# Optimization experiments

Hardware: AMD Instinct MI355X
Metric: run time of the kernel (lower is better)

Reference implementation:

```python
import jax, jax.numpy as jnp
import numpy as np

B, S, D, H = 4, 2048, 1024, 16
DH = D // H


def setup_inputs() -> dict:
    key = jax.random.key(0)
    k1, k2, k3, k4, k5 = jax.random.split(key, 5)
    x = jax.random.normal(k1, (B, S, D), dtype=jnp.float32)
    mask = jnp.tril(jnp.ones((S, S), dtype=bool))  # causal mask
    scale = 1.0 / np.sqrt(D)
    w_qkv = jax.random.normal(k2, (D, 3 * D), dtype=jnp.float32) * scale
    b_qkv = jnp.zeros((3 * D,), dtype=jnp.float32)
    w_out = jax.random.normal(k3, (D, D), dtype=jnp.float32) * scale
    b_out = jnp.zeros((D,), dtype=jnp.float32)
    return {"x": x, "w_qkv": w_qkv, "b_qkv": b_qkv, "w_out": w_out, "b_out": b_out, "mask": mask}


def reference(x, w_qkv, b_qkv, w_out, b_out, mask):
    qkv = jnp.einsum('bsd,de->bse', x, w_qkv) + b_qkv  # (B,S,3D)
    q, k, v = jnp.split(qkv, 3, axis=-1)
    # (B,S,D) -> (B,H,S,DH)
    q = q.reshape(B, S, H, DH).transpose(0, 2, 1, 3)
    k = k.reshape(B, S, H, DH).transpose(0, 2, 1, 3)
    v = v.reshape(B, S, H, DH).transpose(0, 2, 1, 3)
    scores = jnp.einsum('bhqd,bhkd->bhqk', q, k) / jnp.sqrt(jnp.float32(DH))
    scores = jnp.where(mask[None, None, :, :], scores, -jnp.inf)
    attn = jax.nn.softmax(scores, axis=-1)  # dropout p=0.0 -> identity
    out = jnp.einsum('bhqk,bhkd->bhqd', attn, v)
    out = out.transpose(0, 2, 1, 3).reshape(B, S, D)
    return jnp.einsum('bsd,de->bse', out, w_out) + b_out
```

## Files before the change

### kernel.cpp

```cpp
#include <hip/hip_runtime.h>
#include <hip/hip_bf16.h>

typedef unsigned short u16;
typedef __bf16 bf16x8 __attribute__((ext_vector_type(8)));
typedef float f32x4 __attribute__((ext_vector_type(4)));
typedef unsigned short u16x8 __attribute__((ext_vector_type(8)));

__device__ __forceinline__ void async_copy16(void* lds, const void* g) {
  __builtin_amdgcn_global_load_lds(
      (const __attribute__((address_space(1))) unsigned int*)g,
      (__attribute__((address_space(3))) unsigned int*)lds, 16, 0, 0);
}

__device__ __forceinline__ u16 f2bf(float f) {
  __hip_bfloat16 h = __float2bfloat16(f);
  u16 u;
  __builtin_memcpy(&u, &h, 2);
  return u;
}

__device__ __forceinline__ u16 f2bf_rne(float f) {
  unsigned b = __builtin_bit_cast(unsigned, f);
  b += 0x7FFF + ((b >> 16) & 1);
  return (u16)(b >> 16);
}

__device__ __forceinline__ unsigned cvt_pk_bf16(float a, float b) {
  unsigned r;
  asm("v_cvt_pk_bf16_f32 %0, %1, %2" : "=v"(r) : "v"(a), "v"(b));
  return r;
}

__global__ void k_f32_to_bf16(const float* __restrict__ in, u16* __restrict__ out, int n4) {
  int i = blockIdx.x * blockDim.x + threadIdx.x;
  if (i >= n4) return;
  float4 v = ((const float4*)in)[i];
  ushort4 o;
  o.x = f2bf(v.x); o.y = f2bf(v.y); o.z = f2bf(v.z); o.w = f2bf(v.w);
  ((ushort4*)out)[i] = o;
}

__global__ void k_transpose_bf16(const float* __restrict__ in, u16* __restrict__ out, int R, int C) {
  __shared__ float tile[32][33];
  int bx = blockIdx.x * 32;
  int by = blockIdx.y * 32;
  int tx = threadIdx.x & 31, ty = threadIdx.x >> 5;
  for (int i = ty; i < 32; i += 8) tile[i][tx] = in[(size_t)(by + i) * C + bx + tx];
  __syncthreads();
  for (int i = ty; i < 32; i += 8) out[(size_t)(bx + i) * R + by + tx] = f2bf(tile[tx][i]);
}

template <int OUT_BF16>
__global__ __launch_bounds__(256, 2) void k_gemm_bt(
    const u16* __restrict__ A, const u16* __restrict__ Bt,
    const float* __restrict__ bias, void* __restrict__ Cout,
    int M, int N, int K) {
  __shared__ __align__(16) u16 As[128][32];
  __shared__ __align__(16) u16 Bs[128][32];
  const int t = threadIdx.x;
  const int l = t & 63, w = t >> 6;
  const int lr = l & 15, lk = l >> 4;
  const int wr = w >> 1, wc = w & 1;
  const int m0 = blockIdx.x * 128, n0 = blockIdx.y * 128;

  f32x4 acc[4][4] = {};

  for (int k0 = 0; k0 < K; k0 += 32) {
    __syncthreads();
    for (int c = 0; c < 2; ++c) {
      int idx = c * 256 + t;
      int row = idx >> 2, slot = idx & 3;
      int sw = (slot ^ ((row >> 1) & 3)) << 3;
      async_copy16((char*)&As[0][0] + idx * 16, A + (size_t)(m0 + row) * K + k0 + sw);
      async_copy16((char*)&Bs[0][0] + idx * 16, Bt + (size_t)(n0 + row) * K + k0 + sw);
    }
    __syncthreads();
    bf16x8 af[4], bfr[4];
    for (int m = 0; m < 4; ++m) {
      int row = wr * 64 + m * 16 + lr;
      af[m] = *(const bf16x8*)((const char*)&As[0][0] + row * 64 + ((lk ^ ((row >> 1) & 3)) << 4));
    }
    for (int n = 0; n < 4; ++n) {
      int row = wc * 64 + n * 16 + lr;
      bfr[n] = *(const bf16x8*)((const char*)&Bs[0][0] + row * 64 + ((lk ^ ((row >> 1) & 3)) << 4));
    }
    for (int m = 0; m < 4; ++m)
      for (int n = 0; n < 4; ++n)
        acc[m][n] = __builtin_amdgcn_mfma_f32_16x16x32_bf16(af[m], bfr[n], acc[m][n], 0, 0, 0);
  }

  for (int n = 0; n < 4; ++n) {
    int col = n0 + wc * 64 + n * 16 + lr;
    float bv = bias[col];
    for (int m = 0; m < 4; ++m) {
      int rowb = m0 + wr * 64 + m * 16 + lk * 4;
      for (int r = 0; r < 4; ++r) {
        float v = acc[m][n][r] + bv;
        size_t off = (size_t)(rowb + r) * N + col;
        if constexpr (OUT_BF16) ((u16*)Cout)[off] = f2bf(v);
        else ((float*)Cout)[off] = v;
      }
    }
  }
}

__global__ __launch_bounds__(512, 3) void k_attn(
    const u16* __restrict__ QKV,
    u16* __restrict__ O) {
  const int id = blockIdx.x;
  const int bh = (id >> 3) & 63;
  const int e = (id >> 1) & 3;
  const int d = (id & 1) ^ ((id >> 8) & 1);
  const int qt = d ? 7 - e : e;
  const int b = bh >> 4, h = bh & 15;
  const int t = threadIdx.x;
  const int l = t & 63, w = t >> 6;
  const int lr = l & 15, lk = l >> 4;
  constexpr float LG = 0.18033688f;

  __shared__ __align__(16) u16 Ks[2][64][64];
  __shared__ __align__(16) u16 VT[2][64][64];
  __shared__ __align__(16) u16 Pl[8][32][64];

  const u16* Kb0 = QKV + (size_t)b * 2048 * 3072 + 1024 + h * 64;
  const u16* Vb0 = Kb0 + 1024;

  u16x8 vreg;

  auto stageK = [&](int j, int buf) {
    int row = t >> 3, slot = t & 7;
    async_copy16((char*)&Ks[buf][0][0] + t * 16,
                 Kb0 + ((size_t)j * 64 + row) * 3072 + ((slot ^ (row & 7)) << 3));
  };
  auto loadV = [&](int j) {
    vreg = *(const u16x8*)(Vb0 + ((size_t)j * 64 + (t >> 3)) * 3072 + ((t & 7) << 3));
  };
  auto writeV = [&](int buf) {
    int r = t >> 3, dh0 = (t & 7) << 3;
#pragma unroll
    for (int jj = 0; jj < 8; ++jj) {
      int dh = dh0 + jj;
      int phi = (dh & 7) ^ ((dh >> 3) & 7);
      VT[buf][dh][((((r >> 3) ^ phi) & 7) << 3) | (r & 7)] = vreg[jj];
    }
  };

  const int nt = 4 * qt + 4;
  const int q0w = qt * 256 + w * 32;
  const size_t rowQ = (size_t)b * 2048 + q0w;

  bf16x8 qf[2][2];
#pragma unroll
  for (int g = 0; g < 2; ++g)
#pragma unroll
    for (int c = 0; c < 2; ++c)
      qf[g][c] = *(const bf16x8*)(QKV + (rowQ + g * 16 + lr) * 3072 + h * 64 + c * 32 + lk * 8);

  f32x4 acc[2][4] = {};
  float mi[2], li[2];
#pragma unroll
  for (int g = 0; g < 2; ++g) { mi[g] = -__builtin_inff(); li[g] = 0.f; }

  stageK(0, 0);
  loadV(0);
  writeV(0);
  __syncthreads();

  for (int j = 0; j < nt; ++j) {
    const int cur = j & 1;
    const bool more = (j + 1 < nt);
    if (more) { stageK(j + 1, cur ^ 1); loadV(j + 1); }

    f32x4 s[2][4] = {};
    __builtin_amdgcn_s_setprio(1);
#pragma unroll
    for (int c = 0; c < 2; ++c)
#pragma unroll
      for (int n = 0; n < 4; ++n) {
        int row = n * 16 + lr;
        bf16x8 kf = *(const bf16x8*)((const char*)&Ks[cur][0][0] + row * 128 +
                                     ((((c * 4 + lk) ^ (row & 7)) & 7) << 4));
        s[0][n] = __builtin_amdgcn_mfma_f32_16x16x32_bf16(kf, qf[0][c], s[0][n], 0, 0, 0);
        s[1][n] = __builtin_amdgcn_mfma_f32_16x16x32_bf16(kf, qf[1][c], s[1][n], 0, 0, 0);
      }
    __builtin_amdgcn_s_setprio(0);

    if (j * 64 + 63 > q0w) {
      const int kb = j * 64 + lk * 4;
#pragma unroll
      for (int g = 0; g < 2; ++g) {
        const int qq = q0w + g * 16 + lr;
#pragma unroll
        for (int n = 0; n < 4; ++n)
#pragma unroll
          for (int r = 0; r < 4; ++r)
            if (kb + n * 16 + r > qq) s[g][n][r] = -__builtin_inff();
      }
    }

    float tm[2];
#pragma unroll
    for (int g = 0; g < 2; ++g) {
      float m0 = fmaxf(fmaxf(s[g][0][0], s[g][0][1]), fmaxf(s[g][0][2], s[g][0][3]));
      float m1 = fmaxf(fmaxf(s[g][1][0], s[g][1][1]), fmaxf(s[g][1][2], s[g][1][3]));
      float m2 = fmaxf(fmaxf(s[g][2][0], s[g][2][1]), fmaxf(s[g][2][2], s[g][2][3]));
      float m3 = fmaxf(fmaxf(s[g][3][0], s[g][3][1]), fmaxf(s[g][3][2], s[g][3][3]));
      float x = fmaxf(fmaxf(m0, m1), fmaxf(m2, m3));
      x = fmaxf(x, __shfl_xor(x, 16));
      x = fmaxf(x, __shfl_xor(x, 32));
      tm[g] = x;
    }
    if (__any((tm[0] > mi[0] + 64.0f) || (tm[1] > mi[1] + 64.0f))) {
#pragma unroll
      for (int g = 0; g < 2; ++g) {
        float mnew = fmaxf(mi[g], tm[g]);
        float alpha = __builtin_amdgcn_exp2f((mi[g] - mnew) * LG);
        mi[g] = mnew;
        li[g] *= alpha;
        float a0 = __shfl(alpha, lk * 4 + 0);
        float a1 = __shfl(alpha, lk * 4 + 1);
        float a2 = __shfl(alpha, lk * 4 + 2);
        float a3 = __shfl(alpha, lk * 4 + 3);
#pragma unroll
        for (int n = 0; n < 4; ++n) {
          acc[g][n][0] *= a0; acc[g][n][1] *= a1; acc[g][n][2] *= a2; acc[g][n][3] *= a3;
        }
      }
    }

    u16* pw = &Pl[w][0][0];
#pragma unroll
    for (int g = 0; g < 2; ++g) {
      const float mc = -mi[g] * LG;
      float ps = 0.f;
#pragma unroll
      for (int n = 0; n < 4; ++n) {
        float p0 = __builtin_amdgcn_exp2f(fmaf(s[g][n][0], LG, mc));
        float p1 = __builtin_amdgcn_exp2f(fmaf(s[g][n][1], LG, mc));
        float p2 = __builtin_amdgcn_exp2f(fmaf(s[g][n][2], LG, mc));
        float p3 = __builtin_amdgcn_exp2f(fmaf(s[g][n][3], LG, mc));
        ps += (p0 + p1) + (p2 + p3);
        unsigned w0 = cvt_pk_bf16(p0, p1);
        unsigned w1 = cvt_pk_bf16(p2, p3);
        int kc = (n * 2 + (lk >> 1)) ^ (lr & 7);
        *(uint2*)(pw + (g * 16 + lr) * 64 + kc * 8 + (lk & 1) * 4) = make_uint2(w0, w1);
      }
      ps += __shfl_xor(ps, 16);
      ps += __shfl_xor(ps, 32);
      li[g] += ps;
    }

    __builtin_amdgcn_s_setprio(1);
#pragma unroll
    for (int c = 0; c < 2; ++c) {
      bf16x8 pa0 = *(const bf16x8*)(pw + lr * 64 + (((c * 4 + lk) ^ (lr & 7)) << 3));
      bf16x8 pa1 = *(const bf16x8*)(pw + (16 + lr) * 64 + (((c * 4 + lk) ^ (lr & 7)) << 3));
#pragma unroll
      for (int n = 0; n < 4; ++n) {
        int dh = n * 16 + lr;
        int phi = (dh & 7) ^ ((dh >> 3) & 7);
        bf16x8 vf = *(const bf16x8*)((const char*)&VT[cur][0][0] + dh * 128 +
                                     ((((c * 4 + lk) ^ phi) & 7) << 4));
        acc[0][n] = __builtin_amdgcn_mfma_f32_16x16x32_bf16(pa0, vf, acc[0][n], 0, 0, 0);
        acc[1][n] = __builtin_amdgcn_mfma_f32_16x16x32_bf16(pa1, vf, acc[1][n], 0, 0, 0);
      }
    }
    __builtin_amdgcn_s_setprio(0);

    if (more) writeV(cur ^ 1);
    __syncthreads();
  }

#pragma unroll
  for (int g = 0; g < 2; ++g) {
    float l0 = __shfl(li[g], lk * 4 + 0);
    float l1 = __shfl(li[g], lk * 4 + 1);
    float l2 = __shfl(li[g], lk * 4 + 2);
    float l3 = __shfl(li[g], lk * 4 + 3);
    float inv[4] = {1.0f / l0, 1.0f / l1, 1.0f / l2, 1.0f / l3};
#pragma unroll
    for (int r = 0; r < 4; ++r) {
      size_t orow = (rowQ + g * 16 + lk * 4 + r) * 1024 + h * 64;
#pragma unroll
      for (int n = 0; n < 4; ++n) O[orow + n * 16 + lr] = f2bf_rne(acc[g][n][r] * inv[r]);
    }
  }
}

extern "C" void kernel_launch(void* const* d_in, const int* in_sizes, int n_in,
                              void* d_out, int out_size, void* d_ws, size_t ws_size,
                              hipStream_t stream) {
  const float* x = (const float*)d_in[0];
  const float* w_qkv = (const float*)d_in[1];
  const float* b_qkv = (const float*)d_in[2];
  const float* w_out = (const float*)d_in[3];
  const float* b_out = (const float*)d_in[4];

  char* ws = (char*)d_ws;
  u16* X16 = (u16*)(ws);
  u16* WqkvT = (u16*)(ws + 16777216);
  u16* WoutT = (u16*)(ws + 23068672);
  u16* QKVb = (u16*)(ws + 25165824);
  u16* O16 = X16;

  k_f32_to_bf16<<<8192, 256, 0, stream>>>(x, X16, 8388608 / 4);
  k_transpose_bf16<<<dim3(96, 32), 256, 0, stream>>>(w_qkv, WqkvT, 1024, 3072);
  k_transpose_bf16<<<dim3(32, 32), 256, 0, stream>>>(w_out, WoutT, 1024, 1024);
  k_gemm_bt<1><<<dim3(64, 24), 256, 0, stream>>>(X16, WqkvT, b_qkv, QKVb, 8192, 3072, 1024);
  k_attn<<<512, 512, 0, stream>>>(QKVb, O16);
  k_gemm_bt<0><<<dim3(64, 8), 256, 0, stream>>>(O16, WoutT, b_out, d_out, 8192, 1024, 1024);
}
```

Measured before the change: 189.8 us.

## Split score tile per query group, skip fully-masked tiles, raise occupancy bounds

```diff
diff --git a/kernel.cpp b/kernel.cpp
--- a/kernel.cpp
+++ b/kernel.cpp
@@ -51,7 +51,7 @@
 }
 
 template <int OUT_BF16>
-__global__ __launch_bounds__(256, 2) void k_gemm_bt(
+__global__ __launch_bounds__(256, 3) void k_gemm_bt(
     const u16* __restrict__ A, const u16* __restrict__ Bt,
     const float* __restrict__ bias, void* __restrict__ Cout,
     int M, int N, int K) {
@@ -104,7 +104,7 @@
   }
 }
 
-__global__ __launch_bounds__(512, 3) void k_attn(
+__global__ __launch_bounds__(512, 4) void k_attn(
     const u16* __restrict__ QKV,
     u16* __restrict__ O) {
   const int id = blockIdx.x;
@@ -171,101 +171,98 @@
     const bool more = (j + 1 < nt);
     if (more) { stageK(j + 1, cur ^ 1); loadV(j + 1); }
 
-    f32x4 s[2][4] = {};
-    __builtin_amdgcn_s_setprio(1);
-#pragma unroll
-    for (int c = 0; c < 2; ++c)
-#pragma unroll
-      for (int n = 0; n < 4; ++n) {
-        int row = n * 16 + lr;
-        bf16x8 kf = *(const bf16x8*)((const char*)&Ks[cur][0][0] + row * 128 +
-                                     ((((c * 4 + lk) ^ (row & 7)) & 7) << 4));
-        s[0][n] = __builtin_amdgcn_mfma_f32_16x16x32_bf16(kf, qf[0][c], s[0][n], 0, 0, 0);
-        s[1][n] = __builtin_amdgcn_mfma_f32_16x16x32_bf16(kf, qf[1][c], s[1][n], 0, 0, 0);
+    if (j * 64 <= q0w + 31) {
+      u16* pw = &Pl[w][0][0];
+      const bool needmask = (j * 64 + 63 > q0w);
+      const int kb = j * 64 + lk * 4;
+
+#pragma unroll
+      for (int g = 0; g < 2; ++g) {
+        f32x4 s[4] = {};
+        __builtin_amdgcn_s_setprio(1);
+#pragma unroll
+        for (int c = 0; c < 2; ++c)
+#pragma unroll
+          for (int n = 0; n < 4; ++n) {
+            int row = n * 16 + lr;
+            bf16x8 kf = *(const bf16x8*)((const char*)&Ks[cur][0][0] + row * 128 +
+                                         ((((c * 4 + lk) ^ (row & 7)) & 7) << 4));
+            s[n] = __builtin_amdgcn_mfma_f32_16x16x32_bf16(kf, qf[g][c], s[n], 0, 0, 0);
+          }
+        __builtin_amdgcn_s_setprio(0);
+
+        if (needmask) {
+          const int qq = q0w + g * 16 + lr;
+#pragma unroll
+          for (int n = 0; n < 4; ++n)
+#pragma unroll
+            for (int r = 0; r < 4; ++r)
+              if (kb + n * 16 + r > qq) s[n][r] = -__builtin_inff();
+        }
+
+        float tm;
+        {
+          float m0 = fmaxf(fmaxf(s[0][0], s[0][1]), fmaxf(s[0][2], s[0][3]));
+          float m1 = fmaxf(fmaxf(s[1][0], s[1][1]), fmaxf(s[1][2], s[1][3]));
+          float m2 = fmaxf(fmaxf(s[2][0], s[2][1]), fmaxf(s[2][2], s[2][3]));
+          float m3 = fmaxf(fmaxf(s[3][0], s[3][1]), fmaxf(s[3][2], s[3][3]));
+          tm = fmaxf(fmaxf(m0, m1), fmaxf(m2, m3));
+          tm = fmaxf(tm, __shfl_xor(tm, 16));
+          tm = fmaxf(tm, __shfl_xor(tm, 32));
+        }
+        if (__any(tm > mi[g] + 64.0f)) {
+          float mnew = fmaxf(mi[g], tm);
+          float alpha = __builtin_amdgcn_exp2f((mi[g] - mnew) * LG);
+          mi[g] = mnew;
+          li[g] *= alpha;
+          float a0 = __shfl(alpha, lk * 4 + 0);
+          float a1 = __shfl(alpha, lk * 4 + 1);
+          float a2 = __shfl(alpha, lk * 4 + 2);
+          float a3 = __shfl(alpha, lk * 4 + 3);
+#pragma unroll
+          for (int n = 0; n < 4; ++n) {
+            acc[g][n][0] *= a0; acc[g][n][1] *= a1; acc[g][n][2] *= a2; acc[g][n][3] *= a3;
+          }
+        }
+
+        {
+          const float mc = -mi[g] * LG;
+          float ps = 0.f;
+#pragma unroll
+          for (int n = 0; n < 4; ++n) {
+            float p0 = __builtin_amdgcn_exp2f(fmaf(s[n][0], LG, mc));
+            float p1 = __builtin_amdgcn_exp2f(fmaf(s[n][1], LG, mc));
+            float p2 = __builtin_amdgcn_exp2f(fmaf(s[n][2], LG, mc));
+            float p3 = __builtin_amdgcn_exp2f(fmaf(s[n][3], LG, mc));
+            ps += (p0 + p1) + (p2 + p3);
+            unsigned w0 = cvt_pk_bf16(p0, p1);
+            unsigned w1 = cvt_pk_bf16(p2, p3);
+            int kc = (n * 2 + (lk >> 1)) ^ (lr & 7);
+            *(uint2*)(pw + (g * 16 + lr) * 64 + kc * 8 + (lk & 1) * 4) = make_uint2(w0, w1);
+          }
+          ps += __shfl_xor(ps, 16);
+          ps += __shfl_xor(ps, 32);
+          li[g] += ps;
+        }
       }
-    __builtin_amdgcn_s_setprio(0);
-
-    if (j * 64 + 63 > q0w) {
-      const int kb = j * 64 + lk * 4;
-#pragma unroll
-      for (int g = 0; g < 2; ++g) {
-        const int qq = q0w + g * 16 + lr;
-#pragma unroll
-        for (int n = 0; n < 4; ++n)
-#pragma unroll
-          for (int r = 0; r < 4; ++r)
-            if (kb + n * 16 + r > qq) s[g][n][r] = -__builtin_inff();
+
+      __builtin_amdgcn_s_setprio(1);
+#pragma unroll
+      for (int c = 0; c < 2; ++c) {
+        bf16x8 pa0 = *(const bf16x8*)(pw + lr * 64 + (((c * 4 + lk) ^ (lr & 7)) << 3));
+        bf16x8 pa1 = *(const bf16x8*)(pw + (16 + lr) * 64 + (((c * 4 + lk) ^ (lr & 7)) << 3));
+#pragma unroll
+        for (int n = 0; n < 4; ++n) {
+          int dh = n * 16 + lr;
+          int phi = (dh & 7) ^ ((dh >> 3) & 7);
+          bf16x8 vf = *(const bf16x8*)((const char*)&VT[cur][0][0] + dh * 128 +
+                                       ((((c * 4 + lk) ^ phi) & 7) << 4));
+          acc[0][n] = __builtin_amdgcn_mfma_f32_16x16x32_bf16(pa0, vf, acc[0][n], 0, 0, 0);
+          acc[1][n] = __builtin_amdgcn_mfma_f32_16x16x32_bf16(pa1, vf, acc[1][n], 0, 0, 0);
+        }
       }
-    }
-
-    float tm[2];
-#pragma unroll
-    for (int g = 0; g < 2; ++g) {
-      float m0 = fmaxf(fmaxf(s[g][0][0], s[g][0][1]), fmaxf(s[g][0][2], s[g][0][3]));
-      float m1 = fmaxf(fmaxf(s[g][1][0], s[g][1][1]), fmaxf(s[g][1][2], s[g][1][3]));
-      float m2 = fmaxf(fmaxf(s[g][2][0], s[g][2][1]), fmaxf(s[g][2][2], s[g][2][3]));
-      float m3 = fmaxf(fmaxf(s[g][3][0], s[g][3][1]), fmaxf(s[g][3][2], s[g][3][3]));
-      float x = fmaxf(fmaxf(m0, m1), fmaxf(m2, m3));
-      x = fmaxf(x, __shfl_xor(x, 16));
-      x = fmaxf(x, __shfl_xor(x, 32));
-      tm[g] = x;
-    }
-    if (__any((tm[0] > mi[0] + 64.0f) || (tm[1] > mi[1] + 64.0f))) {
-#pragma unroll
-      for (int g = 0; g < 2; ++g) {
-        float mnew = fmaxf(mi[g], tm[g]);
-        float alpha = __builtin_amdgcn_exp2f((mi[g] - mnew) * LG);
-        mi[g] = mnew;
-        li[g] *= alpha;
-        float a0 = __shfl(alpha, lk * 4 + 0);
-        float a1 = __shfl(alpha, lk * 4 + 1);
-        float a2 = __shfl(alpha, lk * 4 + 2);
-        float a3 = __shfl(alpha, lk * 4 + 3);
-#pragma unroll
-        for (int n = 0; n < 4; ++n) {
-          acc[g][n][0] *= a0; acc[g][n][1] *= a1; acc[g][n][2] *= a2; acc[g][n][3] *= a3;
-        }
-      }
-    }
-
-    u16* pw = &Pl[w][0][0];
-#pragma unroll
-    for (int g = 0; g < 2; ++g) {
-      const float mc = -mi[g] * LG;
-      float ps = 0.f;
-#pragma unroll
-      for (int n = 0; n < 4; ++n) {
-        float p0 = __builtin_amdgcn_exp2f(fmaf(s[g][n][0], LG, mc));
-        float p1 = __builtin_amdgcn_exp2f(fmaf(s[g][n][1], LG, mc));
-        float p2 = __builtin_amdgcn_exp2f(fmaf(s[g][n][2], LG, mc));
-        float p3 = __builtin_amdgcn_exp2f(fmaf(s[g][n][3], LG, mc));
-        ps += (p0 + p1) + (p2 + p3);
-        unsigned w0 = cvt_pk_bf16(p0, p1);
-        unsigned w1 = cvt_pk_bf16(p2, p3);
-        int kc = (n * 2 + (lk >> 1)) ^ (lr & 7);
-        *(uint2*)(pw + (g * 16 + lr) * 64 + kc * 8 + (lk & 1) * 4) = make_uint2(w0, w1);
-      }
-      ps += __shfl_xor(ps, 16);
-      ps += __shfl_xor(ps, 32);
-      li[g] += ps;
-    }
-
-    __builtin_amdgcn_s_setprio(1);
-#pragma unroll
-    for (int c = 0; c < 2; ++c) {
-      bf16x8 pa0 = *(const bf16x8*)(pw + lr * 64 + (((c * 4 + lk) ^ (lr & 7)) << 3));
-      bf16x8 pa1 = *(const bf16x8*)(pw + (16 + lr) * 64 + (((c * 4 + lk) ^ (lr & 7)) << 3));
-#pragma unroll
-      for (int n = 0; n < 4; ++n) {
-        int dh = n * 16 + lr;
-        int phi = (dh & 7) ^ ((dh >> 3) & 7);
-        bf16x8 vf = *(const bf16x8*)((const char*)&VT[cur][0][0] + dh * 128 +
-                                     ((((c * 4 + lk) ^ phi) & 7) << 4));
-        acc[0][n] = __builtin_amdgcn_mfma_f32_16x16x32_bf16(pa0, vf, acc[0][n], 0, 0, 0);
-        acc[1][n] = __builtin_amdgcn_mfma_f32_16x16x32_bf16(pa1, vf, acc[1][n], 0, 0, 0);
-      }
-    }
-    __builtin_amdgcn_s_setprio(0);
+      __builtin_amdgcn_s_setprio(0);
+    }
 
     if (more) writeV(cur ^ 1);
     __syncthreads();
```

Result: slower. 274.6 us (+44.7%).
